# Kernel tuning notes

Measured on AMD Instinct MI355X. Metric: run time of the kernel, lower is better.

The kernel has to match this reference:

```python
import jax, jax.numpy as jnp
import numpy as np

NUM_HEADS = 32
HEAD_DIM = 128
NUM_KV_HEADS = 8
SCALE = 0.08838834764831845  # 1/sqrt(128)
T = 2048          # total packed tokens (total_q == total_k in delta branch)
N_SAL = 512       # number of salient rows
NUM_SEQS = 4
EPS = 1e-8
NEG = -1e30


def setup_inputs() -> dict:
    key = jax.random.key(0)
    ks = jax.random.split(key, 5)
    q = jax.random.normal(ks[0], (T, NUM_HEADS, HEAD_DIM), dtype=jnp.float32)
    k = jax.random.normal(ks[1], (T, NUM_KV_HEADS, HEAD_DIM), dtype=jnp.float32)
    v = jax.random.normal(ks[2], (N_SAL, NUM_KV_HEADS, HEAD_DIM), dtype=jnp.float32)
    v_cache = jax.random.normal(ks[3], (T, NUM_KV_HEADS, HEAD_DIM), dtype=jnp.float32)
    c_cache = jax.random.normal(ks[4], (T, NUM_HEADS * HEAD_DIM), dtype=jnp.float32)
    # unique, sorted salient row indices (torch index_copy requires well-defined scatter)
    idx_salient_row = (jnp.arange(N_SAL, dtype=jnp.int64) * (T // N_SAL))
    # 4 equal packed sequences
    cu_seqlens = jnp.array([0, 512, 1024, 1536, 2048], dtype=jnp.int64)
    return {"q": q, "k": k, "v": v, "v_cache": v_cache, "c_cache": c_cache,
            "idx_salient_row": idx_salient_row, "cu_seqlens": cu_seqlens}


def _segment_ids(cu_seqlens, n):
    # seg[i] = which packed sequence row i belongs to (searchsorted right on bounds)
    return jnp.searchsorted(cu_seqlens[1:], jnp.arange(n), side="right")


def _sdpa(q_, k_, v_, seg_q_, seg_k_):
    # GQA: repeat_interleave kv heads to match query heads
    n_rep = q_.shape[1] // k_.shape[1]
    if n_rep > 1:
        k_ = jnp.repeat(k_, n_rep, axis=1)
        v_ = jnp.repeat(v_, n_rep, axis=1)
    scores = jnp.einsum("qhd,khd->hqk", q_, k_) * SCALE  # [H, nq, T]
    allow = (seg_q_[:, None] == seg_k_[None, :])          # [nq, T]
    scores = jnp.where(allow[None, :, :], scores, NEG)
    p = jax.nn.softmax(scores, axis=-1)
    return jnp.einsum("hqk,khd->qhd", p, v_)              # [nq, H, D]


def reference(q, k, v, v_cache, c_cache, idx_salient_row, cu_seqlens):
    total = q.shape[0]
    seg = _segment_ids(cu_seqlens, total)  # seg_q == seg_k (total_q == total_k)

    # delta KV-cache update at salient rows
    v_delta = v - v_cache[idx_salient_row]                      # [n_sal, Hkv, D]
    v_delta_sparse = jnp.zeros_like(k).at[idx_salient_row].set(v_delta)
    v_cache_new = v_cache.at[idx_salient_row].set(v)

    # salient-row full attention against updated cache
    o_salient = _sdpa(q[idx_salient_row], k, v_cache_new, seg[idx_salient_row], seg)
    # sparse delta attention for every row
    delta_c = _sdpa(q, k, v_delta_sparse, seg, seg)

    new_c_flat = c_cache + delta_c.reshape(total, -1)
    new_c_flat = new_c_flat.at[idx_salient_row].set(o_salient.reshape(o_salient.shape[0], -1))

    # cosine similarity between old and new context (early-exit signal)
    num = jnp.sum(c_cache * new_c_flat, axis=-1)
    den_c = jnp.sum(c_cache * c_cache, axis=-1)
    den_n = jnp.sum(new_c_flat * new_c_flat, axis=-1)
    cos_sim = num / (jnp.sqrt(den_c) * jnp.sqrt(den_n) + EPS)

    return new_c_flat.reshape(total, NUM_HEADS, HEAD_DIM), cos_sim
```

## Files before the change

### kernel.cpp

```cpp
#include <hip/hip_runtime.h>
#include <math.h>

#define NUM_HEADS 32
#define HEAD_DIM 128
#define NUM_KV_HEADS 8
#define SCALE 0.08838834764831845f
#define EPS 1e-8f
#define MAX_SEG 512
#define QT 32
#define BLK 512
#define SEGC_MAX 16
#define PB_STRIDE 520
#define PD_STRIDE 136
#define PD_MAX 128
#define SAL_PAD 576
#define SAL_STRIDE 640
#define TLD 130
#define CD (NUM_HEADS * HEAD_DIM)

typedef __bf16 bf16x8 __attribute__((ext_vector_type(8)));
typedef __bf16 bf16x4 __attribute__((ext_vector_type(4)));
typedef float  f32x4  __attribute__((ext_vector_type(4)));

#define MFMA16(a, b, c) __builtin_amdgcn_mfma_f32_16x16x32_bf16((a), (b), (c), 0, 0, 0)

__device__ __forceinline__ int lower_bound_i(const int* __restrict__ a, int n, int key) {
    int lo = 0, hi = n;
    while (lo < hi) { int mid = (lo + hi) >> 1; if (a[mid] < key) lo = mid + 1; else hi = mid; }
    return lo;
}
__device__ __forceinline__ int bsearch_eq(const int* __restrict__ a, int n, int key) {
    int lo = lower_bound_i(a, n, key);
    return (lo < n && a[lo] == key) ? lo : -1;
}

__device__ __forceinline__ void red16(float& xn, float& xc, float& xd) {
#pragma unroll
    for (int m = 1; m <= 8; m <<= 1) {
        xn += __shfl_xor(xn, m, 64);
        xc += __shfl_xor(xc, m, 64);
        xd += __shfl_xor(xd, m, 64);
    }
}

__global__ void prep(const float* __restrict__ k, const float* __restrict__ q,
                     const float* __restrict__ v,
                     const float* __restrict__ vc, const int* __restrict__ idx,
                     const int* __restrict__ cu,
                     __bf16* __restrict__ kb, __bf16* __restrict__ qb,
                     __bf16* __restrict__ vnewT,
                     __bf16* __restrict__ vdScat, __bf16* __restrict__ vdT,
                     int* __restrict__ tinfo, int* __restrict__ rowsal,
                     int T, int Tpad, int n_sal, int n_seq,
                     int nb_conv, int nb_vt, int nb_vd, int use_compact) {
    __shared__ __bf16 tileN[64 * TLD];
    __shared__ __bf16 tileD[64 * TLD];
    __shared__ int sal_of[64];
    const int b = blockIdx.x;
    const int tid = threadIdx.x;

    if (b < nb_conv) {
        const int n8k = T * NUM_KV_HEADS * HEAD_DIM / 8;
        const int n8q = T * NUM_HEADS * HEAD_DIM / 8;
        const int i = b * 256 + tid;
        if (i < n8k) {
            const float4* s4 = (const float4*)(k + (size_t)i * 8);
            float4 a = s4[0], bb = s4[1];
            bf16x8 o;
            o[0]=(__bf16)a.x; o[1]=(__bf16)a.y; o[2]=(__bf16)a.z; o[3]=(__bf16)a.w;
            o[4]=(__bf16)bb.x; o[5]=(__bf16)bb.y; o[6]=(__bf16)bb.z; o[7]=(__bf16)bb.w;
            *(bf16x8*)(kb + (size_t)i * 8) = o;
        } else if (i < n8k + n8q) {
            const int j = i - n8k;
            const float4* s4 = (const float4*)(q + (size_t)j * 8);
            float4 a = s4[0], bb = s4[1];
            bf16x8 o;
            o[0]=(__bf16)a.x; o[1]=(__bf16)a.y; o[2]=(__bf16)a.z; o[3]=(__bf16)a.w;
            o[4]=(__bf16)bb.x; o[5]=(__bf16)bb.y; o[6]=(__bf16)bb.z; o[7]=(__bf16)bb.w;
            *(bf16x8*)(qb + (size_t)j * 8) = o;
        }
        return;
    }
    if (b < nb_conv + nb_vt * NUM_KV_HEADS) {
        const int bb = b - nb_conv;
        const int kv = bb / nb_vt;
        const int r0 = (bb % nb_vt) * 64;
        if (tid < 64) sal_of[tid] = bsearch_eq(idx, n_sal, r0 + tid);
        __syncthreads();
        for (int ii = tid; ii < 64 * 32; ii += 256) {
            int r = ii >> 5, c4 = ii & 31;
            int row = r0 + r;
            float4 fN = {0.f, 0.f, 0.f, 0.f};
            float4 fD = {0.f, 0.f, 0.f, 0.f};
            if (row < T) {
                int s2 = sal_of[r];
                if (s2 >= 0) {
                    float4 a  = *(const float4*)(v  + ((size_t)s2  * NUM_KV_HEADS + kv) * HEAD_DIM + c4 * 4);
                    float4 c  = *(const float4*)(vc + ((size_t)row * NUM_KV_HEADS + kv) * HEAD_DIM + c4 * 4);
                    fN = a;
                    fD.x = a.x - c.x; fD.y = a.y - c.y; fD.z = a.z - c.z; fD.w = a.w - c.w;
                } else {
                    fN = *(const float4*)(vc + ((size_t)row * NUM_KV_HEADS + kv) * HEAD_DIM + c4 * 4);
                }
            }
            __bf16* tn = &tileN[r * TLD + c4 * 4];
            tn[0] = (__bf16)fN.x; tn[1] = (__bf16)fN.y; tn[2] = (__bf16)fN.z; tn[3] = (__bf16)fN.w;
            __bf16* td = &tileD[r * TLD + c4 * 4];
            td[0] = (__bf16)fD.x; td[1] = (__bf16)fD.y; td[2] = (__bf16)fD.z; td[3] = (__bf16)fD.w;
        }
        __syncthreads();
        for (int ii = tid; ii < 128 * 8; ii += 256) {
            int d = ii >> 3, rg = ii & 7;
            int row_out = r0 + rg * 8;
            if (row_out < Tpad) {
                bf16x8 oN, oD;
#pragma unroll
                for (int j = 0; j < 8; j++) {
                    oN[j] = tileN[(rg * 8 + j) * TLD + d];
                    oD[j] = tileD[(rg * 8 + j) * TLD + d];
                }
                *(bf16x8*)(vnewT + ((size_t)kv * HEAD_DIM + d) * Tpad + row_out) = oN;
                if (!use_compact)
                    *(bf16x8*)(vdScat + ((size_t)kv * HEAD_DIM + d) * Tpad + row_out) = oD;
            }
        }
        return;
    }
    if (b < nb_conv + nb_vt * NUM_KV_HEADS + nb_vd * NUM_KV_HEADS) {
        const int bb = b - nb_conv - nb_vt * NUM_KV_HEADS;
        const int kv = bb / nb_vd;
        const int s0 = (bb % nb_vd) * 64;
        for (int ii = tid; ii < 64 * 32; ii += 256) {
            int r = ii >> 5, c4 = ii & 31;
            int s = s0 + r;
            float4 f = {0.f, 0.f, 0.f, 0.f};
            if (s < n_sal) {
                int row = idx[s];
                float4 a  = *(const float4*)(v  + ((size_t)s   * NUM_KV_HEADS + kv) * HEAD_DIM + c4 * 4);
                float4 c2 = *(const float4*)(vc + ((size_t)row * NUM_KV_HEADS + kv) * HEAD_DIM + c4 * 4);
                f.x = a.x - c2.x; f.y = a.y - c2.y; f.z = a.z - c2.z; f.w = a.w - c2.w;
            }
            __bf16* tp = &tileN[r * TLD + c4 * 4];
            tp[0] = (__bf16)f.x; tp[1] = (__bf16)f.y; tp[2] = (__bf16)f.z; tp[3] = (__bf16)f.w;
        }
        __syncthreads();
        for (int ii = tid; ii < 128 * 8; ii += 256) {
            int d = ii >> 3, rg = ii & 7;
            bf16x8 o;
#pragma unroll
            for (int j = 0; j < 8; j++) o[j] = tileN[(rg * 8 + j) * TLD + d];
            *(bf16x8*)(vdT + ((size_t)kv * HEAD_DIM + d) * SAL_STRIDE + s0 + rg * 8) = o;
        }
        return;
    }
    {
        for (int i = tid; i < T; i += 256) rowsal[i] = -1;
        __syncthreads();
        for (int s = tid; s < n_sal; s += 256) rowsal[idx[s]] = s;
        const int NT = T / QT;
        for (int t = tid; t < NT; t += 256) {
            const int r0 = t * QT;
            int a = 0, e = T;
            for (int s = 0; s < n_seq; s++) {
                int x = cu[s], y = cu[s + 1];
                if (r0 >= x && r0 < y) { a = x; e = y; }
            }
            tinfo[t * 4 + 0] = a;
            tinfo[t * 4 + 1] = e;
            tinfo[t * 4 + 2] = lower_bound_i(idx, n_sal, a);
            tinfo[t * 4 + 3] = lower_bound_i(idx, n_sal, e);
        }
    }
}


#define QK_TILE_GEN(ttc) {                                                                  \
    const int t_ = wave * 4 + (ttc);                                                        \
    if (t_ < ntiles) {                                                                      \
        int key_ = seg_start + t_ * 16 + lm;                                                \
        if (key_ >= seg_end) key_ = seg_end - 1;                                            \
        const __bf16* kp_ = kb + ((size_t)key_ * NUM_KV_HEADS + kvh) * HEAD_DIM + quad * 8; \
        const bf16x8 bk0_ = *(const bf16x8*)(kp_);                                          \
        const bf16x8 bk1_ = *(const bf16x8*)(kp_ + 32);                                     \
        const bf16x8 bk2_ = *(const bf16x8*)(kp_ + 64);                                     \
        const bf16x8 bk3_ = *(const bf16x8*)(kp_ + 96);                                     \
        f32x4 a0_ = {0.f,0.f,0.f,0.f}, a1_ = {0.f,0.f,0.f,0.f};                             \
        a0_ = MFMA16(bk0_, aq00, a0_);  a1_ = MFMA16(bk0_, aq10, a1_);                      \
        a0_ = MFMA16(bk1_, aq01, a0_);  a1_ = MFMA16(bk1_, aq11, a1_);                      \
        a0_ = MFMA16(bk2_, aq02, a0_);  a1_ = MFMA16(bk2_, aq12, a1_);                      \
        a0_ = MFMA16(bk3_, aq03, a0_);  a1_ = MFMA16(bk3_, aq13, a1_);                      \
        bf16x4 pk0_, pk1_;                                                                  \
        _Pragma("unroll")                                                                   \
        for (int r_ = 0; r_ < 4; r_++) {                                                    \
            const int kl_ = t_ * 16 + quad * 4 + r_;                                        \
            const bool ok_ = (kl_ < seg_len);                                               \
            float e0_ = ok_ ? __expf(a0_[r_] * SCALE) : 0.f;                                \
            float e1_ = ok_ ? __expf(a1_[r_] * SCALE) : 0.f;                                \
            ps0 += e0_; ps1 += e1_;                                                         \
            pk0_[r_] = (__bf16)e0_; pk1_[r_] = (__bf16)e1_;                                 \
            if (compact && ok_) {                                                           \
                int sr_ = rowsal[seg_start + kl_];                                          \
                if (sr_ >= 0) {                                                             \
                    int c_ = sr_ - s_lo;                                                    \
                    Pd[lm * PD_STRIDE + c_]        = pk0_[r_];                              \
                    Pd[(16 + lm) * PD_STRIDE + c_] = pk1_[r_];                              \
                }                                                                           \
            }                                                                               \
        }                                                                                   \
        *(bf16x4*)&Pb[lm * PB_STRIDE + t_ * 16 + quad * 4] = pk0_;                          \
        *(bf16x4*)&Pb[(16 + lm) * PB_STRIDE + t_ * 16 + quad * 4] = pk1_;                   \
    } }

#define LOADK(buf, t) {                                                                     \
    const __bf16* kn_ = kp + (size_t)(t) * 16 * krow;                                       \
    kk[buf][0] = *(const bf16x8*)(kn_);                                                     \
    kk[buf][1] = *(const bf16x8*)(kn_ + 32);                                                \
    kk[buf][2] = *(const bf16x8*)(kn_ + 64);                                                \
    kk[buf][3] = *(const bf16x8*)(kn_ + 96); }

__global__ __launch_bounds__(BLK, 4)
void attn_mfma(const __bf16* __restrict__ qb, const __bf16* __restrict__ kb,
               const __bf16* __restrict__ vnewT, const __bf16* __restrict__ vdScat,
               const __bf16* __restrict__ vdT,
               const float* __restrict__ c_cache, const int* __restrict__ tinfo,
               const int* __restrict__ rowsal,
               float* __restrict__ out_c, float* __restrict__ cospart,
               int Tpad, int use_compact) {
    const int bid  = blockIdx.x;
    const int kvh  = bid & 7;
    const int rem  = bid >> 3;
    const int h    = kvh * 4 + (rem & 3);
    const int qt   = rem >> 2;
    const int qrow0 = qt * QT;
    const int tid   = threadIdx.x;
    const int wave  = tid >> 6;
    const int lane  = tid & 63;
    const int lm    = lane & 15;
    const int quad  = lane >> 4;

    __shared__ __align__(16) __bf16 Pb[QT * PB_STRIDE];
    __shared__ __align__(16) __bf16 Pd[QT * PD_STRIDE];
    __shared__ float wred[8 * QT];
    __shared__ float linv[QT];
    __shared__ int   salrow[QT];
    __shared__ float cp[8 * 3 * QT];

    const int4 ti = *(const int4*)(tinfo + qt * 4);
    const int seg_start = ti.x, seg_end = ti.y, s_lo = ti.z, s_hi = ti.w;
    const int seg_len = seg_end - seg_start;
    const int nss    = s_hi - s_lo;
    const int ntiles = (seg_len + 15) >> 4;
    const int SEGC   = (seg_len + 31) >> 5;
    const int dim = wave * 16 + lm;
    const bool compact = use_compact && (nss <= PD_MAX);

    if (tid < QT) salrow[tid] = rowsal[qrow0 + tid];
    if (ntiles * 16 < SEGC * 32) {
        for (int ii = tid; ii < QT * 16; ii += BLK) {
            int row = ii >> 4, col = ntiles * 16 + (ii & 15);
            Pb[row * PB_STRIDE + col] = (__bf16)0.f;
        }
    }
    if (compact) {
        const bf16x8 z = {0,0,0,0,0,0,0,0};
        for (int ii = tid; ii < QT * PD_STRIDE / 8; ii += BLK)
            ((bf16x8*)Pd)[ii] = z;
    }

    bf16x8 aq00, aq01, aq02, aq03, aq10, aq11, aq12, aq13;
    {
        const __bf16* qp0 = qb + ((size_t)(qrow0 + lm) * NUM_HEADS + h) * HEAD_DIM + quad * 8;
        const __bf16* qp1 = qb + ((size_t)(qrow0 + 16 + lm) * NUM_HEADS + h) * HEAD_DIM + quad * 8;
        aq00 = *(const bf16x8*)(qp0);      aq01 = *(const bf16x8*)(qp0 + 32);
        aq02 = *(const bf16x8*)(qp0 + 64); aq03 = *(const bf16x8*)(qp0 + 96);
        aq10 = *(const bf16x8*)(qp1);      aq11 = *(const bf16x8*)(qp1 + 32);
        aq12 = *(const bf16x8*)(qp1 + 64); aq13 = *(const bf16x8*)(qp1 + 96);
    }

    const float* cbase = c_cache + (size_t)qrow0 * CD + h * HEAD_DIM + dim;
    float cold[2][4];
#pragma unroll
    for (int rt = 0; rt < 2; rt++)
#pragma unroll
        for (int r = 0; r < 4; r++)
            cold[rt][r] = cbase[(size_t)(rt * 16 + quad * 4 + r) * CD];

    float ps0 = 0.f, ps1 = 0.f;
    if (seg_len == MAX_SEG) {
        const size_t krow = (size_t)NUM_KV_HEADS * HEAD_DIM;
        const __bf16* kp = kb + (size_t)(seg_start + wave * 64 + lm) * krow
                              + (size_t)kvh * HEAD_DIM + quad * 8;
        bf16x8 kk[3][4];
        LOADK(0, 0)
        LOADK(1, 1)
#pragma unroll
        for (int tt = 0; tt < 4; tt++) {
            if (tt + 2 < 4) LOADK((tt + 2) % 3, tt + 2)
            const int cur = tt % 3;
            f32x4 a0_ = {0.f,0.f,0.f,0.f}, a1_ = {0.f,0.f,0.f,0.f};
            a0_ = MFMA16(kk[cur][0], aq00, a0_);  a1_ = MFMA16(kk[cur][0], aq10, a1_);
            a0_ = MFMA16(kk[cur][1], aq01, a0_);  a1_ = MFMA16(kk[cur][1], aq11, a1_);
            a0_ = MFMA16(kk[cur][2], aq02, a0_);  a1_ = MFMA16(kk[cur][2], aq12, a1_);
            a0_ = MFMA16(kk[cur][3], aq03, a0_);  a1_ = MFMA16(kk[cur][3], aq13, a1_);
            const int t_ = wave * 4 + tt;
            bf16x4 pk0_, pk1_;
#pragma unroll
            for (int r_ = 0; r_ < 4; r_++) {
                float e0_ = __expf(a0_[r_] * SCALE);
                float e1_ = __expf(a1_[r_] * SCALE);
                ps0 += e0_; ps1 += e1_;
                pk0_[r_] = (__bf16)e0_; pk1_[r_] = (__bf16)e1_;
            }
            *(bf16x4*)&Pb[lm * PB_STRIDE + t_ * 16 + quad * 4] = pk0_;
            *(bf16x4*)&Pb[(16 + lm) * PB_STRIDE + t_ * 16 + quad * 4] = pk1_;
            if (compact) {
                const int4 sal4 = *(const int4*)&rowsal[seg_start + t_ * 16 + quad * 4];
                const int srl[4] = {sal4.x, sal4.y, sal4.z, sal4.w};
#pragma unroll
                for (int r_ = 0; r_ < 4; r_++) {
                    if (srl[r_] >= 0) {
                        const int c_ = srl[r_] - s_lo;
                        Pd[lm * PD_STRIDE + c_]        = pk0_[r_];
                        Pd[(16 + lm) * PD_STRIDE + c_] = pk1_[r_];
                    }
                }
            }
        }
    } else {
        QK_TILE_GEN(0) QK_TILE_GEN(1) QK_TILE_GEN(2) QK_TILE_GEN(3)
    }
#pragma unroll
    for (int m = 16; m <= 32; m <<= 1) {
        ps0 += __shfl_xor(ps0, m, 64);
        ps1 += __shfl_xor(ps1, m, 64);
    }
    if (quad == 0) {
        wred[wave * QT + lm]      = ps0;
        wred[wave * QT + 16 + lm] = ps1;
    }

    const __bf16* vF = vnewT  + ((size_t)kvh * HEAD_DIM + dim) * Tpad + seg_start + quad * 8;
    const __bf16* vD = vdScat + ((size_t)kvh * HEAD_DIM + dim) * Tpad + seg_start + quad * 8;
    const __bf16* pb0 = &Pb[lm * PB_STRIDE + quad * 8];
    const __bf16* pb1 = &Pb[(16 + lm) * PB_STRIDE + quad * 8];
    bf16x8 fv[4], dv[4];
#pragma unroll
    for (int i = 0; i < 3; i++) {
        fv[i] = *(const bf16x8*)(vF + i * 32);
        if (!compact) dv[i] = *(const bf16x8*)(vD + i * 32);
    }

    __syncthreads();
    if (tid < QT) {
        float s = 0.f;
#pragma unroll
        for (int w = 0; w < 8; w++) s += wred[w * QT + tid];
        linv[tid] = 1.f / s;
    }

    __builtin_amdgcn_s_setprio(1);
    f32x4 accF0 = {0.f,0.f,0.f,0.f}, accF1 = {0.f,0.f,0.f,0.f};
    f32x4 accD0 = {0.f,0.f,0.f,0.f}, accD1 = {0.f,0.f,0.f,0.f};
    if (compact) {
        const int ndc = (nss + 31) >> 5;
        const __bf16* vdb = vdT + ((size_t)kvh * HEAD_DIM + dim) * SAL_STRIDE + s_lo + quad * 8;
        const bool al8 = ((s_lo & 7) == 0);
        for (int dc = 0; dc < ndc; dc++) {
            bf16x8 bvD;
            const __bf16* vp = vdb + dc * 32;
            if (al8) bvD = *(const bf16x8*)vp;
            else {
#pragma unroll
                for (int j = 0; j < 8; j++) bvD[j] = vp[j];
            }
            const bf16x8 aD0 = *(const bf16x8*)&Pd[lm * PD_STRIDE + dc * 32 + quad * 8];
            const bf16x8 aD1 = *(const bf16x8*)&Pd[(16 + lm) * PD_STRIDE + dc * 32 + quad * 8];
            accD0 = MFMA16(aD0, bvD, accD0);
            accD1 = MFMA16(aD1, bvD, accD1);
        }
        if (SEGC == SEGC_MAX) {
            bf16x8 a0c = *(const bf16x8*)(pb0);
            bf16x8 a1c = *(const bf16x8*)(pb1);
#pragma unroll
            for (int cc = 0; cc < SEGC_MAX; cc++) {
                bf16x8 a0n, a1n;
                if (cc + 1 < SEGC_MAX) {
                    a0n = *(const bf16x8*)(pb0 + (cc + 1) * 32);
                    a1n = *(const bf16x8*)(pb1 + (cc + 1) * 32);
                }
                if (cc + 3 < SEGC_MAX)
                    fv[(cc + 3) & 3] = *(const bf16x8*)(vF + (cc + 3) * 32);
                accF0 = MFMA16(a0c, fv[cc & 3], accF0);
                accF1 = MFMA16(a1c, fv[cc & 3], accF1);
                if (cc + 1 < SEGC_MAX) { a0c = a0n; a1c = a1n; }
            }
        } else {
            for (int cc = 0; cc < SEGC; cc++) {
                const bf16x8 bF_ = *(const bf16x8*)(vF + cc * 32);
                accF0 = MFMA16(*(const bf16x8*)(pb0 + cc * 32), bF_, accF0);
                accF1 = MFMA16(*(const bf16x8*)(pb1 + cc * 32), bF_, accF1);
            }
        }
    } else {
        if (SEGC == SEGC_MAX) {
            bf16x8 a0c = *(const bf16x8*)(pb0);
            bf16x8 a1c = *(const bf16x8*)(pb1);
#pragma unroll
            for (int cc = 0; cc < SEGC_MAX; cc++) {
                bf16x8 a0n, a1n;
                if (cc + 1 < SEGC_MAX) {
                    a0n = *(const bf16x8*)(pb0 + (cc + 1) * 32);
                    a1n = *(const bf16x8*)(pb1 + (cc + 1) * 32);
                }
                if (cc + 3 < SEGC_MAX) {
                    fv[(cc + 3) & 3] = *(const bf16x8*)(vF + (cc + 3) * 32);
                    dv[(cc + 3) & 3] = *(const bf16x8*)(vD + (cc + 3) * 32);
                }
                const int cur = cc & 3;
                accF0 = MFMA16(a0c, fv[cur], accF0);
                accF1 = MFMA16(a1c, fv[cur], accF1);
                accD0 = MFMA16(a0c, dv[cur], accD0);
                accD1 = MFMA16(a1c, dv[cur], accD1);
                if (cc + 1 < SEGC_MAX) { a0c = a0n; a1c = a1n; }
            }
        } else {
            for (int cc = 0; cc < SEGC; cc++) {
                const bf16x8 bF_ = *(const bf16x8*)(vF + cc * 32);
                const bf16x8 bD_ = *(const bf16x8*)(vD + cc * 32);
                const bf16x8 a0_ = *(const bf16x8*)(pb0 + cc * 32);
                const bf16x8 a1_ = *(const bf16x8*)(pb1 + cc * 32);
                accF0 = MFMA16(a0_, bF_, accF0);
                accF1 = MFMA16(a1_, bF_, accF1);
                accD0 = MFMA16(a0_, bD_, accD0);
                accD1 = MFMA16(a1_, bD_, accD1);
            }
        }
    }
    __builtin_amdgcn_s_setprio(0);
    __syncthreads();

    float* obase = out_c + (size_t)qrow0 * CD + h * HEAD_DIM + dim;
#pragma unroll
    for (int rt = 0; rt < 2; rt++) {
#pragma unroll
        for (int r = 0; r < 4; r++) {
            const int row = rt * 16 + quad * 4 + r;
            const float c_old = cold[rt][r];
            const float li = linv[row];
            const float aF = (rt == 0) ? accF0[r] : accF1[r];
            const float aD = (rt == 0) ? accD0[r] : accD1[r];
            const float o = (salrow[row] >= 0) ? aF * li : c_old + aD * li;
            obase[(size_t)row * CD] = o;
            float xn = o * c_old, xc = c_old * c_old, xd = o * o;
            red16(xn, xc, xd);
            if (lm == 0) {
                cp[(wave * 3 + 0) * QT + row] = xn;
                cp[(wave * 3 + 1) * QT + row] = xc;
                cp[(wave * 3 + 2) * QT + row] = xd;
            }
        }
    }
    __syncthreads();
    for (int ii = tid; ii < 3 * QT; ii += BLK) {
        int c = ii >> 5, row = ii & 31;
        float s = 0.f;
#pragma unroll
        for (int w = 0; w < 8; w++) s += cp[(w * 3 + c) * QT + row];
        cospart[((size_t)(qrow0 + row) * 3 + c) * NUM_HEADS + h] = s;
    }
}

__global__ void cos_finalize(const float* __restrict__ cospart, float* __restrict__ out_cos, int T) {
    const int lane = threadIdx.x & 63;
    const int row  = blockIdx.x * 4 + (threadIdx.x >> 6);
    if (row >= T) return;
    const float* p = cospart + (size_t)row * (NUM_HEADS * 3);
    float a = p[lane];
    float b = (lane < 32) ? p[64 + lane] : 0.f;
#pragma unroll
    for (int m = 1; m <= 16; m <<= 1) {
        a += __shfl_xor(a, m, 64);
        b += __shfl_xor(b, m, 64);
    }
    float den_c = __shfl(a, 32, 64);
    if (lane == 0) out_cos[row] = a / (sqrtf(den_c) * sqrtf(b) + EPS);
}

extern "C" void kernel_launch(void* const* d_in, const int* in_sizes, int n_in,
                              void* d_out, int out_size, void* d_ws, size_t ws_size,
                              hipStream_t stream) {
    const float* q       = (const float*)d_in[0];
    const float* k       = (const float*)d_in[1];
    const float* v       = (const float*)d_in[2];
    const float* v_cache = (const float*)d_in[3];
    const float* c_cache = (const float*)d_in[4];
    const int*   idx     = (const int*)d_in[5];
    const int*   cu      = (const int*)d_in[6];

    const int T     = in_sizes[0] / CD;
    const int n_sal = in_sizes[5];
    const int n_seq = in_sizes[6] - 1;
    const int Tpad  = T + 32;
    const int NT    = T / QT;
    const int use_compact = (n_sal <= SAL_PAD) ? 1 : 0;

    float* out_c   = (float*)d_out;
    float* out_cos = out_c + (size_t)T * CD;

    char* wsp = (char*)d_ws;
    size_t off = 0;
    __bf16* kb = (__bf16*)(wsp + off);
    off += (((size_t)T * NUM_KV_HEADS * HEAD_DIM * 2) + 255) & ~(size_t)255;
    __bf16* qb = (__bf16*)(wsp + off);
    off += (((size_t)T * NUM_HEADS * HEAD_DIM * 2) + 255) & ~(size_t)255;
    __bf16* vnewT = (__bf16*)(wsp + off);
    off += (((size_t)NUM_KV_HEADS * HEAD_DIM * Tpad * 2) + 255) & ~(size_t)255;
    __bf16* vdScat = (__bf16*)(wsp + off);
    off += (((size_t)NUM_KV_HEADS * HEAD_DIM * Tpad * 2) + 255) & ~(size_t)255;
    __bf16* vdT = (__bf16*)(wsp + off);
    off += (((size_t)NUM_KV_HEADS * HEAD_DIM * SAL_STRIDE * 2) + 255) & ~(size_t)255;
    float* cospart = (float*)(wsp + off);
    off += ((size_t)T * NUM_HEADS * 3 * 4 + 255) & ~(size_t)255;
    int* tinfo = (int*)(wsp + off);
    off += ((size_t)NT * 4 * 4 + 255) & ~(size_t)255;
    int* rowsal = (int*)(wsp + off);
    off += ((size_t)T * 4 + 255) & ~(size_t)255;
    (void)ws_size;

    const int n8_tot  = T * HEAD_DIM * (NUM_KV_HEADS + NUM_HEADS) / 8;
    const int nb_conv = (n8_tot + 255) / 256;
    const int nb_vt   = (Tpad + 63) / 64;
    const int nb_vd   = use_compact ? (SAL_STRIDE / 64) : 0;
    const int nb_tot  = nb_conv + nb_vt * NUM_KV_HEADS + nb_vd * NUM_KV_HEADS + 1;

    prep<<<nb_tot, 256, 0, stream>>>(k, q, v, v_cache, idx, cu, kb, qb, vnewT,
                                     vdScat, vdT, tinfo, rowsal, T, Tpad, n_sal,
                                     n_seq, nb_conv, nb_vt, nb_vd, use_compact);

    attn_mfma<<<NT * NUM_HEADS, BLK, 0, stream>>>(qb, kb, vnewT, vdScat, vdT, c_cache,
                                                  tinfo, rowsal, out_c, cospart,
                                                  Tpad, use_compact);

    cos_finalize<<<(T + 3) / 4, 256, 0, stream>>>(cospart, out_cos, T);
}
```

Measured before the change: 220.1 us.

## Start PV accumulation on own-wave key chunks before barrier; skip unused delta tile work

In the compact path with full segments, each wave now multiplies its own two 32-key chunks of P against V before the block barrier. This overlaps that work with the barrier wait, relying on those P entries having been written by the same wave. The remaining chunks are processed after the barrier, with the register prefetch pipeline replaced by a simple loop that skips the wave's own chunks. The transpose-prep blocks also skip computing, staging and storing the delta tile when the compact path is in use, which removes LDS and global traffic for data that is never read.

```diff
diff --git a/kernel.cpp b/kernel.cpp
--- a/kernel.cpp
+++ b/kernel.cpp
@@ -98,30 +98,35 @@
                     float4 a  = *(const float4*)(v  + ((size_t)s2  * NUM_KV_HEADS + kv) * HEAD_DIM + c4 * 4);
                     float4 c  = *(const float4*)(vc + ((size_t)row * NUM_KV_HEADS + kv) * HEAD_DIM + c4 * 4);
                     fN = a;
-                    fD.x = a.x - c.x; fD.y = a.y - c.y; fD.z = a.z - c.z; fD.w = a.w - c.w;
+                    if (!use_compact) {
+                        fD.x = a.x - c.x; fD.y = a.y - c.y; fD.z = a.z - c.z; fD.w = a.w - c.w;
+                    }
                 } else {
                     fN = *(const float4*)(vc + ((size_t)row * NUM_KV_HEADS + kv) * HEAD_DIM + c4 * 4);
                 }
             }
             __bf16* tn = &tileN[r * TLD + c4 * 4];
             tn[0] = (__bf16)fN.x; tn[1] = (__bf16)fN.y; tn[2] = (__bf16)fN.z; tn[3] = (__bf16)fN.w;
-            __bf16* td = &tileD[r * TLD + c4 * 4];
-            td[0] = (__bf16)fD.x; td[1] = (__bf16)fD.y; td[2] = (__bf16)fD.z; td[3] = (__bf16)fD.w;
+            if (!use_compact) {
+                __bf16* td = &tileD[r * TLD + c4 * 4];
+                td[0] = (__bf16)fD.x; td[1] = (__bf16)fD.y; td[2] = (__bf16)fD.z; td[3] = (__bf16)fD.w;
+            }
         }
         __syncthreads();
         for (int ii = tid; ii < 128 * 8; ii += 256) {
             int d = ii >> 3, rg = ii & 7;
             int row_out = r0 + rg * 8;
             if (row_out < Tpad) {
-                bf16x8 oN, oD;
-#pragma unroll
-                for (int j = 0; j < 8; j++) {
-                    oN[j] = tileN[(rg * 8 + j) * TLD + d];
-                    oD[j] = tileD[(rg * 8 + j) * TLD + d];
+                bf16x8 oN;
+#pragma unroll
+                for (int j = 0; j < 8; j++) oN[j] = tileN[(rg * 8 + j) * TLD + d];
+                *(bf16x8*)(vnewT + ((size_t)kv * HEAD_DIM + d) * Tpad + row_out) = oN;
+                if (!use_compact) {
+                    bf16x8 oD;
+#pragma unroll
+                    for (int j = 0; j < 8; j++) oD[j] = tileD[(rg * 8 + j) * TLD + d];
+                    *(bf16x8*)(vdScat + ((size_t)kv * HEAD_DIM + d) * Tpad + row_out) = oD;
                 }
-                *(bf16x8*)(vnewT + ((size_t)kv * HEAD_DIM + d) * Tpad + row_out) = oN;
-                if (!use_compact)
-                    *(bf16x8*)(vdScat + ((size_t)kv * HEAD_DIM + d) * Tpad + row_out) = oD;
             }
         }
         return;
@@ -253,6 +258,7 @@
     const int SEGC   = (seg_len + 31) >> 5;
     const int dim = wave * 16 + lm;
     const bool compact = use_compact && (nss <= PD_MAX);
+    const bool fullseg = (seg_len == MAX_SEG);
 
     if (tid < QT) salrow[tid] = rowsal[qrow0 + tid];
     if (ntiles * 16 < SEGC * 32) {
@@ -286,7 +292,7 @@
             cold[rt][r] = cbase[(size_t)(rt * 16 + quad * 4 + r) * CD];
 
     float ps0 = 0.f, ps1 = 0.f;
-    if (seg_len == MAX_SEG) {
+    if (fullseg) {
         const size_t krow = (size_t)NUM_KV_HEADS * HEAD_DIM;
         const __bf16* kp = kb + (size_t)(seg_start + wave * 64 + lm) * krow
                               + (size_t)kvh * HEAD_DIM + quad * 8;
@@ -343,11 +349,27 @@
     const __bf16* vD = vdScat + ((size_t)kvh * HEAD_DIM + dim) * Tpad + seg_start + quad * 8;
     const __bf16* pb0 = &Pb[lm * PB_STRIDE + quad * 8];
     const __bf16* pb1 = &Pb[(16 + lm) * PB_STRIDE + quad * 8];
+
+    f32x4 accF0 = {0.f,0.f,0.f,0.f}, accF1 = {0.f,0.f,0.f,0.f};
+    f32x4 accD0 = {0.f,0.f,0.f,0.f}, accD1 = {0.f,0.f,0.f,0.f};
     bf16x8 fv[4], dv[4];
-#pragma unroll
-    for (int i = 0; i < 3; i++) {
-        fv[i] = *(const bf16x8*)(vF + i * 32);
-        if (!compact) dv[i] = *(const bf16x8*)(vD + i * 32);
+
+    if (compact) {
+        if (fullseg) {
+            const int c0 = wave * 2;
+            const bf16x8 f0_ = *(const bf16x8*)(vF + c0 * 32);
+            const bf16x8 f1_ = *(const bf16x8*)(vF + c0 * 32 + 32);
+            accF0 = MFMA16(*(const bf16x8*)(pb0 + c0 * 32), f0_, accF0);
+            accF1 = MFMA16(*(const bf16x8*)(pb1 + c0 * 32), f0_, accF1);
+            accF0 = MFMA16(*(const bf16x8*)(pb0 + c0 * 32 + 32), f1_, accF0);
+            accF1 = MFMA16(*(const bf16x8*)(pb1 + c0 * 32 + 32), f1_, accF1);
+        }
+    } else {
+#pragma unroll
+        for (int i = 0; i < 3; i++) {
+            fv[i] = *(const bf16x8*)(vF + i * 32);
+            dv[i] = *(const bf16x8*)(vD + i * 32);
+        }
     }
 
     __syncthreads();
@@ -359,8 +381,6 @@
     }
 
     __builtin_amdgcn_s_setprio(1);
-    f32x4 accF0 = {0.f,0.f,0.f,0.f}, accF1 = {0.f,0.f,0.f,0.f};
-    f32x4 accD0 = {0.f,0.f,0.f,0.f}, accD1 = {0.f,0.f,0.f,0.f};
     if (compact) {
         const int ndc = (nss + 31) >> 5;
         const __bf16* vdb = vdT + ((size_t)kvh * HEAD_DIM + dim) * SAL_STRIDE + s_lo + quad * 8;
@@ -378,21 +398,13 @@
             accD0 = MFMA16(aD0, bvD, accD0);
             accD1 = MFMA16(aD1, bvD, accD1);
         }
-        if (SEGC == SEGC_MAX) {
-            bf16x8 a0c = *(const bf16x8*)(pb0);
-            bf16x8 a1c = *(const bf16x8*)(pb1);
+        if (fullseg) {
 #pragma unroll
             for (int cc = 0; cc < SEGC_MAX; cc++) {
-                bf16x8 a0n, a1n;
-                if (cc + 1 < SEGC_MAX) {
-                    a0n = *(const bf16x8*)(pb0 + (cc + 1) * 32);
-                    a1n = *(const bf16x8*)(pb1 + (cc + 1) * 32);
-                }
-                if (cc + 3 < SEGC_MAX)
-                    fv[(cc + 3) & 3] = *(const bf16x8*)(vF + (cc + 3) * 32);
-                accF0 = MFMA16(a0c, fv[cc & 3], accF0);
-                accF1 = MFMA16(a1c, fv[cc & 3], accF1);
-                if (cc + 1 < SEGC_MAX) { a0c = a0n; a1c = a1n; }
+                if ((cc >> 1) == wave) continue;
+                const bf16x8 bF_ = *(const bf16x8*)(vF + cc * 32);
+                accF0 = MFMA16(*(const bf16x8*)(pb0 + cc * 32), bF_, accF0);
+                accF1 = MFMA16(*(const bf16x8*)(pb1 + cc * 32), bF_, accF1);
             }
         } else {
             for (int cc = 0; cc < SEGC; cc++) {
```

After: 225.2 us. 2.3% more time.
